# Kernel tuning notes

Hardware: AMD Instinct MI355X
Metric: run time of the kernel (lower is better)

## Reference

```python
import jax, jax.numpy as jnp
import numpy as np

NT, NC, D = 20000, 80000, 256
SLOPE = 0.01  # torch F.leaky_relu default negative_slope


def _lrelu(x):
    return jnp.where(x >= 0, x, SLOPE * x)


def setup_inputs() -> dict:
    key = jax.random.key(0)
    ks = jax.random.split(key, 20)
    sc = 1.0 / np.sqrt(D)

    def W(k):
        return jax.random.normal(k, (D, D), jnp.float32) * sc

    return {
        "feat_table": jax.random.normal(ks[0], (NT, D), jnp.float32),
        "feat_column": jax.random.normal(ks[1], (NC, D), jnp.float32),
        "W_t2c": W(ks[2]), "b_t2c": jnp.zeros((D,), jnp.float32),
        "W_c2t": W(ks[3]), "b_c2t": jnp.zeros((D,), jnp.float32),
        "W_c2c": W(ks[4]), "b_c2c": jnp.zeros((D,), jnp.float32),
        "W_t2t": W(ks[5]), "b_t2t": jnp.zeros((D,), jnp.float32),
        "W_h": W(ks[6]), "b_h": jnp.zeros((D,), jnp.float32),
        "src_t2c": jax.random.randint(ks[7], (320000,), 0, NT, jnp.int32),
        "dst_t2c": jax.random.randint(ks[8], (320000,), 0, NC, jnp.int32),
        "src_c2t": jax.random.randint(ks[9], (320000,), 0, NC, jnp.int32),
        "dst_c2t": jax.random.randint(ks[10], (320000,), 0, NT, jnp.int32),
        "src_c2c": jax.random.randint(ks[11], (640000,), 0, NC, jnp.int32),
        "dst_c2c": jax.random.randint(ks[12], (640000,), 0, NC, jnp.int32),
        "src_t2t": jax.random.randint(ks[13], (160000,), 0, NT, jnp.int32),
        "dst_t2t": jax.random.randint(ks[14], (160000,), 0, NT, jnp.int32),
    }


def _mean_agg(Wh, src, dst, n_dst):
    # copy_u + mean: gather src messages, segment-mean into dst nodes
    s = jax.ops.segment_sum(Wh[src], dst, num_segments=n_dst)  # [n_dst, D]
    c = jax.ops.segment_sum(jnp.ones(src.shape, Wh.dtype), dst, num_segments=n_dst)
    return s / jnp.maximum(c, 1.0)[:, None]


def reference(feat_table, feat_column,
              W_t2c, b_t2c, W_c2t, b_c2t, W_c2c, b_c2c, W_t2t, b_t2t,
              W_h, b_h,
              src_t2c, dst_t2c, src_c2t, dst_c2t,
              src_c2c, dst_c2c, src_t2t, dst_t2t):
    # per-etype Linear + leaky_relu on source-node features
    Wh_t2c = _lrelu(feat_table @ W_t2c.T + b_t2c)
    Wh_c2t = _lrelu(feat_column @ W_c2t.T + b_c2t)
    Wh_c2c = _lrelu(feat_column @ W_c2c.T + b_c2c)
    Wh_t2t = _lrelu(feat_table @ W_t2t.T + b_t2t)

    # per-etype mean aggregation, then cross-etype 'mean' (2 etypes per ntype)
    h_table = 0.5 * (_mean_agg(Wh_c2t, src_c2t, dst_c2t, NT)
                     + _mean_agg(Wh_t2t, src_t2t, dst_t2t, NT))
    h_column = 0.5 * (_mean_agg(Wh_t2c, src_t2c, dst_t2c, NC)
                      + _mean_agg(Wh_c2c, src_c2c, dst_c2c, NC))

    out_table = _lrelu(h_table @ W_h.T + b_h) + feat_table
    out_column = _lrelu(h_column @ W_h.T + b_h) + feat_column
    return out_table, out_column
```

## Files before the change

kernel.cpp:

```cpp
#include <hip/hip_runtime.h>

#define D 256
#define SLOPE 0.01f

#define BSH 9
#define BSZ 512
#define NBMAX 160
#define EPB 8192

typedef __attribute__((ext_vector_type(8))) short bf16x8;
typedef __attribute__((ext_vector_type(4))) float f32x4;

__device__ __forceinline__ float bfbits2f(unsigned int hi) {
  return __builtin_bit_cast(float, hi);
}
__device__ __forceinline__ unsigned short f2bf(float f) {
  unsigned u = __builtin_bit_cast(unsigned, f);
  u += 0x7fffu + ((u >> 16) & 1u);
  return (unsigned short)(u >> 16);
}
__device__ __forceinline__ float lrelu(float x) {
  return (x >= 0.f) ? x : SLOPE * x;
}

__device__ __forceinline__ void gld_lds16(const void* g, void* l) {
  __builtin_amdgcn_global_load_lds(
      (const __attribute__((address_space(1))) unsigned int*)g,
      (__attribute__((address_space(3))) unsigned int*)l, 16, 0, 0);
}

__global__ void cast5_kernel(const float* w0, const float* w1, const float* w2,
                             const float* w3, const float* w4,
                             unsigned short* o0, unsigned short* o1,
                             unsigned short* o2, unsigned short* o3,
                             unsigned short* o4) {
  int a = blockIdx.y;
  const float* in = a == 0 ? w0 : a == 1 ? w1 : a == 2 ? w2 : a == 3 ? w3 : w4;
  unsigned short* out = a == 0 ? o0 : a == 1 ? o1 : a == 2 ? o2 : a == 3 ? o3 : o4;
  int i = blockIdx.x * blockDim.x + threadIdx.x;
  float4 v = ((const float4*)in)[i];
  ushort4 o;
  o.x = f2bf(v.x); o.y = f2bf(v.y); o.z = f2bf(v.z); o.w = f2bf(v.w);
  ((ushort4*)out)[i] = o;
}


__device__ __forceinline__ void stage_A(unsigned short* Xs,
                                        const unsigned short* __restrict__ A,
                                        int M, int mblk) {
  const int t = threadIdx.x;
  const int w = t >> 6, lane = t & 63;
#pragma unroll
  for (int i = 0; i < 8; i++) {
    const int m = (i * 4 + w) * 2 + (lane >> 5);
    int row = mblk + m;
    if (row > M - 1) row = M - 1;
    const int jsrc = (lane & 31) ^ (m & 7);
    gld_lds16(A + (size_t)row * D + jsrc * 8, &Xs[(i * 4 + w) * 512]);
  }
}

__device__ __forceinline__ void stage_A_f32(unsigned short* Xs,
                                            const float* __restrict__ A,
                                            int M, int mblk) {
  const int t = threadIdx.x;
#pragma unroll
  for (int c = 0; c < 8; c++) {
    const int chunk = c * 256 + t;
    const int m = chunk >> 5, jg = chunk & 31;
    int row = mblk + m;
    if (row > M - 1) row = M - 1;
    const float* gp = A + (size_t)row * D + jg * 8;
    float4 v0 = *(const float4*)gp;
    float4 v1 = *(const float4*)(gp + 4);
    uint4 pk;
    pk.x = (unsigned)f2bf(v0.x) | ((unsigned)f2bf(v0.y) << 16);
    pk.y = (unsigned)f2bf(v0.z) | ((unsigned)f2bf(v0.w) << 16);
    pk.z = (unsigned)f2bf(v1.x) | ((unsigned)f2bf(v1.y) << 16);
    pk.w = (unsigned)f2bf(v1.z) | ((unsigned)f2bf(v1.w) << 16);
    *(uint4*)&Xs[(m * 32 + (jg ^ (m & 7))) * 8] = pk;
  }
}

template <int MODE, bool SYNC>
__device__ __forceinline__ void gemm_compute(
    const unsigned short* Xs, const unsigned short* __restrict__ B,
    const float* __restrict__ bias, const float* __restrict__ residual,
    unsigned short* __restrict__ outb, float* __restrict__ outf, int M,
    int mblk) {
  const int t = threadIdx.x;
  const int w = t >> 6, lane = t & 63;
  const int fr = lane & 15;
  const int jb = lane >> 4;

  bf16x8 wf[4][8];
  {
    const unsigned short* wp = B + (size_t)(w * 64 + fr) * D + jb * 8;
#pragma unroll
    for (int nt = 0; nt < 4; nt++)
#pragma unroll
      for (int k0 = 0; k0 < 8; k0++)
        wf[nt][k0] = *(const bf16x8*)(wp + nt * 16 * D + k0 * 32);
  }

  if (SYNC) {
    asm volatile("s_waitcnt vmcnt(0)" ::: "memory");
    __syncthreads();
  }

  f32x4 acc[4][4];
#pragma unroll
  for (int i = 0; i < 4; i++)
#pragma unroll
    for (int j = 0; j < 4; j++) acc[i][j] = (f32x4){0.f, 0.f, 0.f, 0.f};

  const int r = fr & 7;
#pragma unroll
  for (int k0 = 0; k0 < 8; k0++) {
    bf16x8 xf[4];
#pragma unroll
    for (int mt = 0; mt < 4; mt++) {
      const int ml = mt * 16 + fr;
      xf[mt] = *(const bf16x8*)&Xs[ml * 256 + (((k0 * 4 + jb) ^ r) * 8)];
    }
#pragma unroll
    for (int mt = 0; mt < 4; mt++)
#pragma unroll
      for (int nt = 0; nt < 4; nt++)
        acc[mt][nt] = __builtin_amdgcn_mfma_f32_16x16x32_bf16(
            wf[nt][k0], xf[mt], acc[mt][nt], 0, 0, 0);
  }

  const int n0 = w * 64 + jb * 4;
  float4 bv[4];
#pragma unroll
  for (int nt = 0; nt < 4; nt++) bv[nt] = *(const float4*)&bias[n0 + nt * 16];

#pragma unroll
  for (int mt = 0; mt < 4; mt++) {
    const int m = mblk + mt * 16 + fr;
    if (m < M) {
      if (MODE == 1) {
        float4 rv[4];
#pragma unroll
        for (int nt = 0; nt < 4; nt++)
          rv[nt] = *(const float4*)&residual[(size_t)m * D + n0 + nt * 16];
#pragma unroll
        for (int nt = 0; nt < 4; nt++) {
          float4 o;
          o.x = lrelu(acc[mt][nt][0] + bv[nt].x) + rv[nt].x;
          o.y = lrelu(acc[mt][nt][1] + bv[nt].y) + rv[nt].y;
          o.z = lrelu(acc[mt][nt][2] + bv[nt].z) + rv[nt].z;
          o.w = lrelu(acc[mt][nt][3] + bv[nt].w) + rv[nt].w;
          *(float4*)&outf[(size_t)m * D + n0 + nt * 16] = o;
        }
      } else {
#pragma unroll
        for (int nt = 0; nt < 4; nt++) {
          ushort4 o;
          o.x = f2bf(lrelu(acc[mt][nt][0] + bv[nt].x));
          o.y = f2bf(lrelu(acc[mt][nt][1] + bv[nt].y));
          o.z = f2bf(lrelu(acc[mt][nt][2] + bv[nt].z));
          o.w = f2bf(lrelu(acc[mt][nt][3] + bv[nt].w));
          *(ushort4*)&outb[(size_t)m * D + n0 + nt * 16] = o;
        }
      }
    }
  }
}

__global__ __launch_bounds__(256, 2) void gemm0_pair(
    const float* __restrict__ A0, const float* __restrict__ A1,
    const unsigned short* __restrict__ B00, const unsigned short* __restrict__ B01,
    const unsigned short* __restrict__ B10, const unsigned short* __restrict__ B11,
    const float* b00, const float* b01, const float* b10, const float* b11,
    unsigned short* o00, unsigned short* o01, unsigned short* o10,
    unsigned short* o11, int M0, int M1) {
  __shared__ __attribute__((aligned(16))) unsigned short Xs[64 * 256];
  int a = blockIdx.y;
  const float* A = a ? A1 : A0;
  int M = a ? M1 : M0;
  int mblk = blockIdx.x * 64;
  if (mblk >= M) return;
  stage_A_f32(Xs, A, M, mblk);
  gemm_compute<0, true>(Xs, a ? B10 : B00, a ? b10 : b00, nullptr,
                        a ? o10 : o00, nullptr, M, mblk);
  gemm_compute<0, false>(Xs, a ? B11 : B01, a ? b11 : b01, nullptr,
                         a ? o11 : o01, nullptr, M, mblk);
}

__global__ __launch_bounds__(256, 2) void gemm1_dual(
    const unsigned short* __restrict__ A0, const unsigned short* __restrict__ A1,
    const unsigned short* __restrict__ Bw, const float* bh,
    const float* __restrict__ r0, const float* __restrict__ r1,
    float* __restrict__ o0, float* __restrict__ o1, int M0, int M1) {
  __shared__ __attribute__((aligned(16))) unsigned short Xs[64 * 256];
  int a = blockIdx.y;
  const unsigned short* A = a ? A1 : A0;
  int M = a ? M1 : M0;
  int mblk = blockIdx.x * 64;
  if (mblk >= M) return;
  stage_A(Xs, A, M, mblk);
  gemm_compute<1, true>(Xs, Bw, bh, a ? r1 : r0, nullptr, a ? o1 : o0, M, mblk);
}

__global__ __launch_bounds__(256) void bucketCount_kernel(
    const int* d0, int n0, const int* d1, int n1, const int* d2, int n2,
    const int* d3, int n3, int* __restrict__ bcnt) {
  int a = blockIdx.y;
  const int* dst = a == 0 ? d0 : a == 1 ? d1 : a == 2 ? d2 : d3;
  int n = a == 0 ? n0 : a == 1 ? n1 : a == 2 ? n2 : n3;
  int blk = blockIdx.x;
  if (blk * EPB >= n) return;
  int t = threadIdx.x;
  __shared__ int cnt[NBMAX];
  if (t < NBMAX) cnt[t] = 0;
  __syncthreads();
  int i0 = blk * EPB + t;
#pragma unroll 4
  for (int it = 0; it < EPB / 256; it++) {
    int i = i0 + it * 256;
    if (i < n) atomicAdd(&cnt[dst[i] >> BSH], 1);
  }
  __syncthreads();
  if (t < NBMAX && cnt[t]) atomicAdd(&bcnt[a * NBMAX + t], cnt[t]);
}

__global__ __launch_bounds__(256) void bucketScan_kernel(
    const int* __restrict__ bcnt, int* __restrict__ bbase,
    int* o0, int n0, int e0, int* o1, int n1, int e1,
    int* o2, int n2, int e2, int* o3, int n3, int e3) {
  __shared__ int s[256];
  int t = threadIdx.x;
  for (int a = 0; a < 4; a++) {
    int v = (t < NBMAX) ? bcnt[a * NBMAX + t] : 0;
    s[t] = v;
    __syncthreads();
    for (int off = 1; off < 256; off <<= 1) {
      int u = (t >= off) ? s[t - off] : 0;
      __syncthreads();
      s[t] += u;
      __syncthreads();
    }
    if (t < NBMAX)
      bbase[a * (NBMAX + 1) + t] = s[t] - v;
    else if (t == NBMAX)
      bbase[a * (NBMAX + 1) + NBMAX] = s[NBMAX - 1];
    __syncthreads();
  }
  if (t == 0) { o0[n0] = e0; o1[n1] = e1; o2[n2] = e2; o3[n3] = e3; }
}

__global__ __launch_bounds__(256) void bucketA_kernel(
    const int* s0, const int* d0, int n0, unsigned* t0,
    const int* s1, const int* d1, int n1, unsigned* t1,
    const int* s2, const int* d2, int n2, unsigned* t2,
    const int* s3, const int* d3, int n3, unsigned* t3,
    const int* __restrict__ bbase, int* __restrict__ bcur) {
  int a = blockIdx.y;
  const int* src = a == 0 ? s0 : a == 1 ? s1 : a == 2 ? s2 : s3;
  const int* dst = a == 0 ? d0 : a == 1 ? d1 : a == 2 ? d2 : d3;
  int n = a == 0 ? n0 : a == 1 ? n1 : a == 2 ? n2 : n3;
  unsigned* temp = a == 0 ? t0 : a == 1 ? t1 : a == 2 ? t2 : t3;

  int blk = blockIdx.x;
  if (blk * EPB >= n) return;
  int t = threadIdx.x;
  __shared__ int cnt[NBMAX];
  __shared__ int lbase[NBMAX];
  if (t < NBMAX) cnt[t] = 0;
  __syncthreads();

  int i0 = blk * EPB + t;
#pragma unroll 4
  for (int it = 0; it < EPB / 256; it++) {
    int i = i0 + it * 256;
    if (i < n) atomicAdd(&cnt[dst[i] >> BSH], 1);
  }
  __syncthreads();
  if (t < NBMAX) {
    int c = cnt[t];
    int g = c ? atomicAdd(&bcur[a * NBMAX + t], c) : 0;
    lbase[t] = g + bbase[a * (NBMAX + 1) + t];
    cnt[t] = 0;
  }
  __syncthreads();
#pragma unroll 4
  for (int it = 0; it < EPB / 256; it++) {
    int i = i0 + it * 256;
    if (i < n) {
      int d = dst[i];
      int b = d >> BSH;
      int rk = atomicAdd(&cnt[b], 1);
      temp[lbase[b] + rk] = ((unsigned)src[i] << BSH) | (unsigned)(d & (BSZ - 1));
    }
  }
}

__global__ __launch_bounds__(256) void bucketFinal_kernel(
    const unsigned* t0, int* o0, int* e0, int m0,
    const unsigned* t1, int* o1, int* e1, int m1,
    const unsigned* t2, int* o2, int* e2, int m2,
    const unsigned* t3, int* o3, int* e3, int m3,
    const int* __restrict__ bbase) {
  int a = blockIdx.y;
  const unsigned* temp = a == 0 ? t0 : a == 1 ? t1 : a == 2 ? t2 : t3;
  int* offs = a == 0 ? o0 : a == 1 ? o1 : a == 2 ? o2 : o3;
  int* elist = a == 0 ? e0 : a == 1 ? e1 : a == 2 ? e2 : e3;
  int nn = a == 0 ? m0 : a == 1 ? m1 : a == 2 ? m2 : m3;

  int nb = (nn + BSZ - 1) >> BSH;
  int b = blockIdx.x;
  if (b >= nb) return;
  int lo = bbase[a * (NBMAX + 1) + b];
  int hi = bbase[a * (NBMAX + 1) + b + 1];
  int t = threadIdx.x;

  __shared__ int cnt[BSZ];
  __shared__ int psum[BSZ];
  __shared__ int sm[256];
  cnt[t] = 0; cnt[t + 256] = 0;
  __syncthreads();
  for (int i = lo + t; i < hi; i += 256)
    atomicAdd(&cnt[temp[i] & (BSZ - 1)], 1);
  __syncthreads();
  int c0 = cnt[2 * t], c1 = cnt[2 * t + 1];
  int s = c0 + c1;
  sm[t] = s;
  __syncthreads();
  for (int off = 1; off < 256; off <<= 1) {
    int u = (t >= off) ? sm[t - off] : 0;
    __syncthreads();
    sm[t] += u;
    __syncthreads();
  }
  int ex = sm[t] - s;
  psum[2 * t] = ex;
  psum[2 * t + 1] = ex + c0;
  cnt[2 * t] = 0; cnt[2 * t + 1] = 0;
  __syncthreads();

  int node0 = b << BSH;
  if (node0 + 2 * t < nn) offs[node0 + 2 * t] = lo + psum[2 * t];
  if (node0 + 2 * t + 1 < nn) offs[node0 + 2 * t + 1] = lo + psum[2 * t + 1];

  for (int i = lo + t; i < hi; i += 256) {
    unsigned v = temp[i];
    int d = v & (BSZ - 1);
    int rk = atomicAdd(&cnt[d], 1);
    elist[lo + psum[d] + rk] = (int)(v >> BSH);
  }
}

__device__ __forceinline__ void add8(float* acc, uint4 p) {
  acc[0] += bfbits2f(p.x << 16);
  acc[1] += bfbits2f(p.x & 0xffff0000u);
  acc[2] += bfbits2f(p.y << 16);
  acc[3] += bfbits2f(p.y & 0xffff0000u);
  acc[4] += bfbits2f(p.z << 16);
  acc[5] += bfbits2f(p.z & 0xffff0000u);
  acc[6] += bfbits2f(p.w << 16);
  acc[7] += bfbits2f(p.w & 0xffff0000u);
}

__global__ __launch_bounds__(256) void aggregate_kernel(
    const unsigned short* __restrict__ WhA, const int* __restrict__ offsA,
    const int* __restrict__ elistA, const unsigned short* __restrict__ WhB,
    const int* __restrict__ offsB, const int* __restrict__ elistB,
    unsigned short* __restrict__ hout, int n) {
  int wave = (blockIdx.x * 256 + threadIdx.x) >> 6;
  int lane = threadIdx.x & 63;
  if (wave >= n) return;
  int half = lane >> 5;
  int l32 = lane & 31;
  size_t coff = (size_t)l32 * 8;

  float accA[8] = {0, 0, 0, 0, 0, 0, 0, 0};
  float accB[8] = {0, 0, 0, 0, 0, 0, 0, 0};
  float scA, scB;

  {
    int e0 = offsA[wave], e1 = offsA[wave + 1];
    scA = 0.5f / fmaxf((float)(e1 - e0), 1.0f);
    int e = e0;
    for (; e + 8 <= e1; e += 8) {
      int s0 = elistA[e + half];
      int s1 = elistA[e + 2 + half];
      int s2 = elistA[e + 4 + half];
      int s3 = elistA[e + 6 + half];
      uint4 p0 = *(const uint4*)(WhA + (size_t)s0 * D + coff);
      uint4 p1 = *(const uint4*)(WhA + (size_t)s1 * D + coff);
      uint4 p2 = *(const uint4*)(WhA + (size_t)s2 * D + coff);
      uint4 p3 = *(const uint4*)(WhA + (size_t)s3 * D + coff);
      add8(accA, p0); add8(accA, p1); add8(accA, p2); add8(accA, p3);
    }
    for (; e + 2 <= e1; e += 2) {
      int s0 = elistA[e + half];
      uint4 p0 = *(const uint4*)(WhA + (size_t)s0 * D + coff);
      add8(accA, p0);
    }
    if (e < e1 && half == 0) {
      int s0 = elistA[e];
      uint4 p0 = *(const uint4*)(WhA + (size_t)s0 * D + coff);
      add8(accA, p0);
    }
  }
  {
    int e0 = offsB[wave], e1 = offsB[wave + 1];
    scB = 0.5f / fmaxf((float)(e1 - e0), 1.0f);
    int e = e0;
    for (; e + 8 <= e1; e += 8) {
      int s0 = elistB[e + half];
      int s1 = elistB[e + 2 + half];
      int s2 = elistB[e + 4 + half];
      int s3 = elistB[e + 6 + half];
      uint4 p0 = *(const uint4*)(WhB + (size_t)s0 * D + coff);
      uint4 p1 = *(const uint4*)(WhB + (size_t)s1 * D + coff);
      uint4 p2 = *(const uint4*)(WhB + (size_t)s2 * D + coff);
      uint4 p3 = *(const uint4*)(WhB + (size_t)s3 * D + coff);
      add8(accB, p0); add8(accB, p1); add8(accB, p2); add8(accB, p3);
    }
    for (; e + 2 <= e1; e += 2) {
      int s0 = elistB[e + half];
      uint4 p0 = *(const uint4*)(WhB + (size_t)s0 * D + coff);
      add8(accB, p0);
    }
    if (e < e1 && half == 0) {
      int s0 = elistB[e];
      uint4 p0 = *(const uint4*)(WhB + (size_t)s0 * D + coff);
      add8(accB, p0);
    }
  }

  float h[8];
#pragma unroll
  for (int j = 0; j < 8; j++) {
    h[j] = accA[j] * scA + accB[j] * scB;
    h[j] += __shfl_down(h[j], 32);
  }
  if (half == 0) {
    uint4 o;
    o.x = (unsigned)f2bf(h[0]) | ((unsigned)f2bf(h[1]) << 16);
    o.y = (unsigned)f2bf(h[2]) | ((unsigned)f2bf(h[3]) << 16);
    o.z = (unsigned)f2bf(h[4]) | ((unsigned)f2bf(h[5]) << 16);
    o.w = (unsigned)f2bf(h[6]) | ((unsigned)f2bf(h[7]) << 16);
    *(uint4*)(hout + (size_t)wave * D + coff) = o;
  }
}

extern "C" void kernel_launch(void* const* d_in, const int* in_sizes, int n_in,
                              void* d_out, int out_size, void* d_ws,
                              size_t ws_size, hipStream_t stream) {
  const float* feat_table = (const float*)d_in[0];
  const float* feat_column = (const float*)d_in[1];
  const float* Wsrc[5] = {(const float*)d_in[2], (const float*)d_in[4],
                          (const float*)d_in[6], (const float*)d_in[8],
                          (const float*)d_in[10]};
  const float* b_t2c = (const float*)d_in[3];
  const float* b_c2t = (const float*)d_in[5];
  const float* b_c2c = (const float*)d_in[7];
  const float* b_t2t = (const float*)d_in[9];
  const float* b_h = (const float*)d_in[11];
  const int* src_t2c = (const int*)d_in[12];
  const int* dst_t2c = (const int*)d_in[13];
  const int* src_c2t = (const int*)d_in[14];
  const int* dst_c2t = (const int*)d_in[15];
  const int* src_c2c = (const int*)d_in[16];
  const int* dst_c2c = (const int*)d_in[17];
  const int* src_t2t = (const int*)d_in[18];
  const int* dst_t2t = (const int*)d_in[19];

  const int NT = in_sizes[0] / D;
  const int NC = in_sizes[1] / D;
  const int E_t2c = in_sizes[12], E_c2t = in_sizes[14];
  const int E_c2c = in_sizes[16], E_t2t = in_sizes[18];

  char* ws = (char*)d_ws;
  size_t cur = 0;
  auto alloc = [&](size_t bytes) -> void* {
    void* p = ws + cur;
    cur += (bytes + 255) & ~(size_t)255;
    return p;
  };
  unsigned short* Wb[5];
  for (int i = 0; i < 5; i++) Wb[i] = (unsigned short*)alloc((size_t)D * D * 2);
  size_t scratchA = sizeof(unsigned) * ((size_t)E_c2t + E_t2t + E_t2c + E_c2c);
  size_t scratchB = (size_t)(NT + NC) * D * 2;
  unsigned short* scr = (unsigned short*)alloc(scratchA > scratchB ? scratchA
                                                                   : scratchB);
  unsigned short* Wh_t2c = (unsigned short*)alloc((size_t)NT * D * 2);
  unsigned short* Wh_c2t = (unsigned short*)alloc((size_t)NC * D * 2);
  unsigned short* Wh_c2c = (unsigned short*)alloc((size_t)NC * D * 2);
  unsigned short* Wh_t2t = (unsigned short*)alloc((size_t)NT * D * 2);
  int* bcnt = (int*)alloc(sizeof(int) * 2 * 4 * NBMAX);
  int* bcur = bcnt + 4 * NBMAX;
  int* bbase = (int*)alloc(sizeof(int) * 4 * (NBMAX + 1));
  int* off_c2t = (int*)alloc(sizeof(int) * (NT + 1));
  int* off_t2t = (int*)alloc(sizeof(int) * (NT + 1));
  int* off_t2c = (int*)alloc(sizeof(int) * (NC + 1));
  int* off_c2c = (int*)alloc(sizeof(int) * (NC + 1));
  int* el_c2t = (int*)alloc(sizeof(int) * E_c2t);
  int* el_t2t = (int*)alloc(sizeof(int) * E_t2t);
  int* el_t2c = (int*)alloc(sizeof(int) * E_t2c);
  int* el_c2c = (int*)alloc(sizeof(int) * E_c2c);

  unsigned* tp_c2t = (unsigned*)scr;
  unsigned* tp_t2t = tp_c2t + E_c2t;
  unsigned* tp_t2c = tp_t2t + E_t2t;
  unsigned* tp_c2c = tp_t2c + E_t2c;
  unsigned short* h_tab = scr;
  unsigned short* h_col = scr + (size_t)NT * D;

  hipMemsetAsync(bcnt, 0, sizeof(int) * 2 * 4 * NBMAX, stream);

  {
    dim3 g((D * D / 4 + 255) / 256, 5);
    cast5_kernel<<<g, 256, 0, stream>>>(Wsrc[0], Wsrc[1], Wsrc[2], Wsrc[3],
                                        Wsrc[4], Wb[0], Wb[1], Wb[2], Wb[3],
                                        Wb[4]);
  }

  {
    dim3 g((max(NT, NC) + 63) / 64, 2);
    gemm0_pair<<<g, 256, 0, stream>>>(
        feat_table, feat_column, Wb[0], Wb[3], Wb[1], Wb[2], b_t2c, b_t2t,
        b_c2t, b_c2c, Wh_t2c, Wh_t2t, Wh_c2t, Wh_c2c, NT, NC);
  }

  int Emax = max(max(E_c2t, E_t2t), max(E_t2c, E_c2c));
  {
    dim3 g((Emax + EPB - 1) / EPB, 4);
    bucketCount_kernel<<<g, 256, 0, stream>>>(dst_c2t, E_c2t, dst_t2t, E_t2t,
                                              dst_t2c, E_t2c, dst_c2c, E_c2c,
                                              bcnt);
  }
  bucketScan_kernel<<<1, 256, 0, stream>>>(
      bcnt, bbase, off_c2t, NT, E_c2t, off_t2t, NT, E_t2t, off_t2c, NC, E_t2c,
      off_c2c, NC, E_c2c);
  {
    dim3 g((Emax + EPB - 1) / EPB, 4);
    bucketA_kernel<<<g, 256, 0, stream>>>(
        src_c2t, dst_c2t, E_c2t, tp_c2t, src_t2t, dst_t2t, E_t2t, tp_t2t,
        src_t2c, dst_t2c, E_t2c, tp_t2c, src_c2c, dst_c2c, E_c2c, tp_c2c,
        bbase, bcur);
  }
  {
    int nbmax = (max(NT, NC) + BSZ - 1) >> BSH;
    dim3 g(nbmax, 4);
    bucketFinal_kernel<<<g, 256, 0, stream>>>(
        tp_c2t, off_c2t, el_c2t, NT, tp_t2t, off_t2t, el_t2t, NT,
        tp_t2c, off_t2c, el_t2c, NC, tp_c2c, off_c2c, el_c2c, NC, bbase);
  }

  aggregate_kernel<<<(NC + 3) / 4, 256, 0, stream>>>(
      Wh_t2c, off_t2c, el_t2c, Wh_c2c, off_c2c, el_c2c, h_col, NC);
  aggregate_kernel<<<(NT + 3) / 4, 256, 0, stream>>>(
      Wh_c2t, off_c2t, el_c2t, Wh_t2t, off_t2t, el_t2t, h_tab, NT);

  float* out_tab = (float*)d_out;
  float* out_col = out_tab + (size_t)NT * D;
  {
    dim3 g((max(NT, NC) + 63) / 64, 2);
    gemm1_dual<<<g, 256, 0, stream>>>(h_tab, h_col, Wb[4], b_h, feat_table,
                                      feat_column, out_tab, out_col, NT, NC);
  }
}
```

Measured before the change: 533.8 us.

## Split GEMM output columns into two passes and flatten grid to avoid empty blocks

The GEMM compute now handles 32 output columns per wave in two passes rather than 64 at once. This halves the register-resident weight fragments and accumulators, so launch bounds can be raised from 2 to 3 blocks per SM. The 2D grid, where table blocks beyond NT returned early, is replaced with a flat 1D grid of nbT+nbC blocks, removing the idle launches. In exchange, the shared-memory A tile is read twice and weight loads are split, with a possible extra load-latency stall at the start of the second pass.

```diff
diff --git a/kernel.cpp b/kernel.cpp
--- a/kernel.cpp
+++ b/kernel.cpp
@@ -83,7 +83,7 @@
 }
 
 template <int MODE, bool SYNC>
-__device__ __forceinline__ void gemm_compute(
+__device__ __forceinline__ void gemm_compute32(
     const unsigned short* Xs, const unsigned short* __restrict__ B,
     const float* __restrict__ bias, const float* __restrict__ residual,
     unsigned short* __restrict__ outb, float* __restrict__ outf, int M,
@@ -92,116 +92,119 @@
   const int w = t >> 6, lane = t & 63;
   const int fr = lane & 15;
   const int jb = lane >> 4;
-
-  bf16x8 wf[4][8];
-  {
-    const unsigned short* wp = B + (size_t)(w * 64 + fr) * D + jb * 8;
-#pragma unroll
-    for (int nt = 0; nt < 4; nt++)
-#pragma unroll
-      for (int k0 = 0; k0 < 8; k0++)
-        wf[nt][k0] = *(const bf16x8*)(wp + nt * 16 * D + k0 * 32);
-  }
-
-  if (SYNC) {
-    asm volatile("s_waitcnt vmcnt(0)" ::: "memory");
-    __syncthreads();
-  }
-
-  f32x4 acc[4][4];
-#pragma unroll
-  for (int i = 0; i < 4; i++)
-#pragma unroll
-    for (int j = 0; j < 4; j++) acc[i][j] = (f32x4){0.f, 0.f, 0.f, 0.f};
-
   const int r = fr & 7;
-#pragma unroll
-  for (int k0 = 0; k0 < 8; k0++) {
-    bf16x8 xf[4];
+
+#pragma unroll
+  for (int c = 0; c < 2; c++) {
+    const int colbase = c * 128 + w * 32;
+    bf16x8 wf[2][8];
+    {
+      const unsigned short* wp = B + (size_t)(colbase + fr) * D + jb * 8;
+#pragma unroll
+      for (int nt = 0; nt < 2; nt++)
+#pragma unroll
+        for (int k0 = 0; k0 < 8; k0++)
+          wf[nt][k0] = *(const bf16x8*)(wp + nt * 16 * D + k0 * 32);
+    }
+
+    if (SYNC && c == 0) {
+      asm volatile("s_waitcnt vmcnt(0)" ::: "memory");
+      __syncthreads();
+    }
+
+    f32x4 acc[4][2];
+#pragma unroll
+    for (int i = 0; i < 4; i++)
+#pragma unroll
+      for (int j = 0; j < 2; j++) acc[i][j] = (f32x4){0.f, 0.f, 0.f, 0.f};
+
+#pragma unroll
+    for (int k0 = 0; k0 < 8; k0++) {
+      bf16x8 xf[4];
+#pragma unroll
+      for (int mt = 0; mt < 4; mt++) {
+        const int ml = mt * 16 + fr;
+        xf[mt] = *(const bf16x8*)&Xs[ml * 256 + (((k0 * 4 + jb) ^ r) * 8)];
+      }
+#pragma unroll
+      for (int mt = 0; mt < 4; mt++)
+#pragma unroll
+        for (int nt = 0; nt < 2; nt++)
+          acc[mt][nt] = __builtin_amdgcn_mfma_f32_16x16x32_bf16(
+              wf[nt][k0], xf[mt], acc[mt][nt], 0, 0, 0);
+    }
+
+    const int n0 = colbase + jb * 4;
+    float4 bv[2];
+#pragma unroll
+    for (int nt = 0; nt < 2; nt++) bv[nt] = *(const float4*)&bias[n0 + nt * 16];
+
 #pragma unroll
     for (int mt = 0; mt < 4; mt++) {
-      const int ml = mt * 16 + fr;
-      xf[mt] = *(const bf16x8*)&Xs[ml * 256 + (((k0 * 4 + jb) ^ r) * 8)];
-    }
-#pragma unroll
-    for (int mt = 0; mt < 4; mt++)
-#pragma unroll
-      for (int nt = 0; nt < 4; nt++)
-        acc[mt][nt] = __builtin_amdgcn_mfma_f32_16x16x32_bf16(
-            wf[nt][k0], xf[mt], acc[mt][nt], 0, 0, 0);
-  }
-
-  const int n0 = w * 64 + jb * 4;
-  float4 bv[4];
-#pragma unroll
-  for (int nt = 0; nt < 4; nt++) bv[nt] = *(const float4*)&bias[n0 + nt * 16];
-
-#pragma unroll
-  for (int mt = 0; mt < 4; mt++) {
-    const int m = mblk + mt * 16 + fr;
-    if (m < M) {
-      if (MODE == 1) {
-        float4 rv[4];
-#pragma unroll
-        for (int nt = 0; nt < 4; nt++)
-          rv[nt] = *(const float4*)&residual[(size_t)m * D + n0 + nt * 16];
-#pragma unroll
-        for (int nt = 0; nt < 4; nt++) {
-          float4 o;
-          o.x = lrelu(acc[mt][nt][0] + bv[nt].x) + rv[nt].x;
-          o.y = lrelu(acc[mt][nt][1] + bv[nt].y) + rv[nt].y;
-          o.z = lrelu(acc[mt][nt][2] + bv[nt].z) + rv[nt].z;
-          o.w = lrelu(acc[mt][nt][3] + bv[nt].w) + rv[nt].w;
-          *(float4*)&outf[(size_t)m * D + n0 + nt * 16] = o;
-        }
-      } else {
-#pragma unroll
-        for (int nt = 0; nt < 4; nt++) {
-          ushort4 o;
-          o.x = f2bf(lrelu(acc[mt][nt][0] + bv[nt].x));
-          o.y = f2bf(lrelu(acc[mt][nt][1] + bv[nt].y));
-          o.z = f2bf(lrelu(acc[mt][nt][2] + bv[nt].z));
-          o.w = f2bf(lrelu(acc[mt][nt][3] + bv[nt].w));
-          *(ushort4*)&outb[(size_t)m * D + n0 + nt * 16] = o;
+      const int m = mblk + mt * 16 + fr;
+      if (m < M) {
+        if (MODE == 1) {
+          float4 rv[2];
+#pragma unroll
+          for (int nt = 0; nt < 2; nt++)
+            rv[nt] = *(const float4*)&residual[(size_t)m * D + n0 + nt * 16];
+#pragma unroll
+          for (int nt = 0; nt < 2; nt++) {
+            float4 o;
+            o.x = lrelu(acc[mt][nt][0] + bv[nt].x) + rv[nt].x;
+            o.y = lrelu(acc[mt][nt][1] + bv[nt].y) + rv[nt].y;
+            o.z = lrelu(acc[mt][nt][2] + bv[nt].z) + rv[nt].z;
+            o.w = lrelu(acc[mt][nt][3] + bv[nt].w) + rv[nt].w;
+            *(float4*)&outf[(size_t)m * D + n0 + nt * 16] = o;
+          }
+        } else {
+#pragma unroll
+          for (int nt = 0; nt < 2; nt++) {
+            ushort4 o;
+            o.x = f2bf(lrelu(acc[mt][nt][0] + bv[nt].x));
+            o.y = f2bf(lrelu(acc[mt][nt][1] + bv[nt].y));
+            o.z = f2bf(lrelu(acc[mt][nt][2] + bv[nt].z));
+            o.w = f2bf(lrelu(acc[mt][nt][3] + bv[nt].w));
+            *(ushort4*)&outb[(size_t)m * D + n0 + nt * 16] = o;
+          }
         }
       }
     }
   }
 }
 
-__global__ __launch_bounds__(256, 2) void gemm0_pair(
+__global__ __launch_bounds__(256, 3) void gemm0_pair(
     const float* __restrict__ A0, const float* __restrict__ A1,
     const unsigned short* __restrict__ B00, const unsigned short* __restrict__ B01,
     const unsigned short* __restrict__ B10, const unsigned short* __restrict__ B11,
     const float* b00, const float* b01, const float* b10, const float* b11,
     unsigned short* o00, unsigned short* o01, unsigned short* o10,
-    unsigned short* o11, int M0, int M1) {
+    unsigned short* o11, int M0, int M1, int nbT) {
   __shared__ __attribute__((aligned(16))) unsigned short Xs[64 * 256];
-  int a = blockIdx.y;
+  const int a = (blockIdx.x >= nbT) ? 1 : 0;
   const float* A = a ? A1 : A0;
-  int M = a ? M1 : M0;
-  int mblk = blockIdx.x * 64;
-  if (mblk >= M) return;
+  const int M = a ? M1 : M0;
+  const int mblk = (a ? (blockIdx.x - nbT) : blockIdx.x) * 64;
   stage_A_f32(Xs, A, M, mblk);
-  gemm_compute<0, true>(Xs, a ? B10 : B00, a ? b10 : b00, nullptr,
-                        a ? o10 : o00, nullptr, M, mblk);
-  gemm_compute<0, false>(Xs, a ? B11 : B01, a ? b11 : b01, nullptr,
-                         a ? o11 : o01, nullptr, M, mblk);
-}
-
-__global__ __launch_bounds__(256, 2) void gemm1_dual(
+  gemm_compute32<0, true>(Xs, a ? B10 : B00, a ? b10 : b00, nullptr,
+                          a ? o10 : o00, nullptr, M, mblk);
+  gemm_compute32<0, false>(Xs, a ? B11 : B01, a ? b11 : b01, nullptr,
+                           a ? o11 : o01, nullptr, M, mblk);
+}
+
+__global__ __launch_bounds__(256, 3) void gemm1_dual(
     const unsigned short* __restrict__ A0, const unsigned short* __restrict__ A1,
     const unsigned short* __restrict__ Bw, const float* bh,
     const float* __restrict__ r0, const float* __restrict__ r1,
-    float* __restrict__ o0, float* __restrict__ o1, int M0, int M1) {
+    float* __restrict__ o0, float* __restrict__ o1, int M0, int M1, int nbT) {
   __shared__ __attribute__((aligned(16))) unsigned short Xs[64 * 256];
-  int a = blockIdx.y;
+  const int a = (blockIdx.x >= nbT) ? 1 : 0;
   const unsigned short* A = a ? A1 : A0;
-  int M = a ? M1 : M0;
-  int mblk = blockIdx.x * 64;
-  if (mblk >= M) return;
+  const int M = a ? M1 : M0;
+  const int mblk = (a ? (blockIdx.x - nbT) : blockIdx.x) * 64;
   stage_A(Xs, A, M, mblk);
-  gemm_compute<1, true>(Xs, Bw, bh, a ? r1 : r0, nullptr, a ? o1 : o0, M, mblk);
+  gemm_compute32<1, true>(Xs, Bw, bh, a ? r1 : r0, nullptr, a ? o1 : o0, M,
+                          mblk);
 }
 
 __global__ __launch_bounds__(256) void bucketCount_kernel(
@@ -520,12 +523,11 @@
                                         Wb[4]);
   }
 
-  {
-    dim3 g((max(NT, NC) + 63) / 64, 2);
-    gemm0_pair<<<g, 256, 0, stream>>>(
-        feat_table, feat_column, Wb[0], Wb[3], Wb[1], Wb[2], b_t2c, b_t2t,
-        b_c2t, b_c2c, Wh_t2c, Wh_t2t, Wh_c2t, Wh_c2c, NT, NC);
-  }
+  const int nbT = (NT + 63) / 64, nbC = (NC + 63) / 64;
+
+  gemm0_pair<<<nbT + nbC, 256, 0, stream>>>(
+      feat_table, feat_column, Wb[0], Wb[3], Wb[1], Wb[2], b_t2c, b_t2t,
+      b_c2t, b_c2c, Wh_t2c, Wh_t2t, Wh_c2t, Wh_c2c, NT, NC, nbT);
 
   int Emax = max(max(E_c2t, E_t2t), max(E_t2c, E_c2c));
   {
@@ -559,9 +561,7 @@
 
   float* out_tab = (float*)d_out;
   float* out_col = out_tab + (size_t)NT * D;
-  {
-    dim3 g((max(NT, NC) + 63) / 64, 2);
-    gemm1_dual<<<g, 256, 0, stream>>>(h_tab, h_col, Wb[4], b_h, feat_table,
-                                      feat_column, out_tab, out_col, NT, NC);
-  }
-}
+  gemm1_dual<<<nbT + nbC, 256, 0, stream>>>(h_tab, h_col, Wb[4], b_h,
+                                            feat_table, feat_column, out_tab,
+                                            out_col, NT, NC, nbT);
+}
```

New measurement: 576.2 us. +8.0%, slower.
